# Performance work log

Hardware: AMD Instinct MI355X
Metric: run time of the kernel (lower is better)

The kernel has to match this reference:

```python
import jax, jax.numpy as jnp
import numpy as np

B, S, H = 1, 2048, 2048
NH = 16
HS = H // NH  # 128
NEG = -65504.0  # fp16 min used as additive mask value


def setup_inputs() -> dict:
    key = jax.random.key(0)
    k1, k2, k3, k4, k5 = jax.random.split(key, 5)
    hidden_states = jax.random.normal(k1, (B, S, H), dtype=jnp.float32)
    # causal left-to-right mask: 1 where attention allowed
    ltor_mask = jnp.tril(jnp.ones((S, S), dtype=jnp.float32))[None, None, :, :]
    W_qkv = jax.random.normal(k2, (H, 3 * H), dtype=jnp.float32) * (1.0 / np.sqrt(H))
    b_qkv = jax.random.normal(k3, (3 * H,), dtype=jnp.float32) * 0.01
    W_dense = jax.random.normal(k4, (H, H), dtype=jnp.float32) * (1.0 / np.sqrt(H))
    b_dense = jax.random.normal(k5, (H,), dtype=jnp.float32) * 0.01
    return {"hidden_states": hidden_states, "ltor_mask": ltor_mask,
            "W_qkv": W_qkv, "b_qkv": b_qkv, "W_dense": W_dense, "b_dense": b_dense}


def reference(hidden_states, ltor_mask, W_qkv, b_qkv, W_dense, b_dense):
    b, s, h = hidden_states.shape
    # fused QKV projection, then split along last dim (matches split_tensor_along_last_dim)
    qkv = hidden_states @ W_qkv + b_qkv  # [b, s, 3h]
    q, k, v = jnp.split(qkv, 3, axis=-1)
    q = q.reshape(b, s, NH, HS)
    k = k.reshape(b, s, NH, HS)
    v = v.reshape(b, s, NH, HS)
    scale = 1.0 / np.sqrt(HS)  # softmax_scale=None -> 1/sqrt(headdim)
    scores = jnp.einsum('bqhd,bkhd->bhqk', q, k) * scale
    scores = scores + NEG * (1.0 - ltor_mask)  # additive mask, [b,1,s,s] broadcast over heads
    probs = jax.nn.softmax(scores, axis=-1)
    ctx = jnp.einsum('bhqk,bkhd->bqhd', probs, v).reshape(b, s, h)
    out = ctx @ W_dense + b_dense  # output_dropout is identity in eval
    return out
```

## Files before the change

### kernel.cpp

```cpp
#include <hip/hip_runtime.h>
#include <math.h>

#define S_LEN 2048
#define HDIM  2048
#define NHEAD 16
#define HSZ   128
#define H3    6144

typedef __attribute__((ext_vector_type(8))) short bf16x8;
typedef __attribute__((ext_vector_type(4))) float f32x4;

__device__ inline ushort f2bf(float f) {
    union { float f; unsigned u; } c; c.f = f;
    unsigned u = c.u;
    return (ushort)((u + 0x7fffu + ((u >> 16) & 1u)) >> 16);
}
__device__ inline ushort f2bf_trunc(float f) {
    union { float f; unsigned u; } c; c.f = f;
    return (ushort)(c.u >> 16);
}

__global__ __launch_bounds__(256) void prep(
    const float* __restrict__ X,    ushort* __restrict__ Xb,
    const float* __restrict__ Wqkv, ushort* __restrict__ Wqt,
    const float* __restrict__ Wd,   ushort* __restrict__ Wdt)
{
    __shared__ ushort t[64][66];
    const int bid = blockIdx.x;
    const int tid = threadIdx.x;

    if (bid < 4096) {
        int i = bid * 1024 + tid * 4;
        float4 v = *(const float4*)(X + i);
        ushort4 o;
        o.x = f2bf(v.x); o.y = f2bf(v.y); o.z = f2bf(v.z); o.w = f2bf(v.w);
        *(ushort4*)(Xb + i) = o;
        return;
    }

    const float* W; ushort* Wt; int K, N, n0, k0;
    if (bid < 7168) {
        const int b = bid - 4096;
        W = Wqkv; Wt = Wqt; K = HDIM; N = H3;
        n0 = (b % 96) * 64; k0 = (b / 96) * 64;
    } else {
        const int b = bid - 7168;
        W = Wd; Wt = Wdt; K = HDIM; N = HDIM;
        n0 = (b % 32) * 64; k0 = (b / 32) * 64;
    }
    const int tx = tid & 15;
    const int ty = tid >> 4;
    #pragma unroll
    for (int p = 0; p < 4; p++) {
        const int k = p * 16 + ty;
        float4 v = *(const float4*)(&W[(size_t)(k0 + k) * N + n0 + tx * 4]);
        t[k][tx * 4 + 0] = f2bf(v.x);
        t[k][tx * 4 + 1] = f2bf(v.y);
        t[k][tx * 4 + 2] = f2bf(v.z);
        t[k][tx * 4 + 3] = f2bf(v.w);
    }
    __syncthreads();
    #pragma unroll
    for (int p = 0; p < 4; p++) {
        const int n = p * 16 + ty;
        ushort4 o;
        o.x = t[tx * 4 + 0][n];
        o.y = t[tx * 4 + 1][n];
        o.z = t[tx * 4 + 2][n];
        o.w = t[tx * 4 + 3][n];
        *(ushort4*)(&Wt[(size_t)(n0 + n) * K + k0 + tx * 4]) = o;
    }
}

__global__ __launch_bounds__(256) void transpose_v(const ushort* __restrict__ qkvb,
                                                   ushort* __restrict__ Vtb) {
    __shared__ ushort t[64][66];
    const int s0 = blockIdx.x * 64;
    const int d0 = blockIdx.y * 64;
    const int tx = threadIdx.x & 15;
    const int ty = threadIdx.x >> 4;
    #pragma unroll
    for (int p = 0; p < 4; p++) {
        const int s = p * 16 + ty;
        ushort4 v = *(const ushort4*)(&qkvb[(size_t)(s0 + s) * H3 + 2 * HDIM + d0 + tx * 4]);
        *(ushort4*)(&t[s][tx * 4]) = v;
    }
    __syncthreads();
    #pragma unroll
    for (int p = 0; p < 4; p++) {
        const int d = p * 16 + ty;
        ushort4 o;
        o.x = t[tx * 4 + 0][d];
        o.y = t[tx * 4 + 1][d];
        o.z = t[tx * 4 + 2][d];
        o.w = t[tx * 4 + 3][d];
        *(ushort4*)(&Vtb[(size_t)(d0 + d) * S_LEN + s0 + tx * 4]) = o;
    }
}

template <bool BF16_OUT>
__global__ __launch_bounds__(256) void gemm_bt_bias(
    const ushort* __restrict__ A, const ushort* __restrict__ Bt,
    const float* __restrict__ bias, float* __restrict__ C,
    ushort* __restrict__ Cb, int M, int N, int K)
{
    __shared__ ushort sA[2 * 128 * 32];
    __shared__ ushort sB[2 * 128 * 32];

    const int tid  = threadIdx.x;
    const int m0   = blockIdx.y * 128;
    const int n0   = blockIdx.x * 128;
    const int w    = tid >> 6;
    const int lane = tid & 63;
    const int quad = lane >> 4;
    const int l16  = lane & 15;
    const int wr   = (w >> 1) * 64;
    const int wc   = (w & 1) * 64;

    f32x4 acc[4][4] = {};

    for (int k0 = 0; k0 < K; k0 += 64) {
        #pragma unroll
        for (int iss = 0; iss < 4; iss++) {
            const int li  = iss * 256 + tid;
            const int c   = li >> 9;
            const int row = (li >> 2) & 127;
            const int kc  = (li & 3) * 8;
            const ushort* ga = A  + (size_t)(m0 + row) * K + k0 + c * 32 + kc;
            const ushort* gb = Bt + (size_t)(n0 + row) * K + k0 + c * 32 + kc;
            __builtin_amdgcn_global_load_lds(
                (const __attribute__((address_space(1))) void*)ga,
                (__attribute__((address_space(3))) void*)(sA + li * 8), 16, 0, 0);
            __builtin_amdgcn_global_load_lds(
                (const __attribute__((address_space(1))) void*)gb,
                (__attribute__((address_space(3))) void*)(sB + li * 8), 16, 0, 0);
        }
        __syncthreads();

        #pragma unroll
        for (int c = 0; c < 2; c++) {
            bf16x8 af[4], bq[4];
            #pragma unroll
            for (int i = 0; i < 4; i++)
                af[i] = *(const bf16x8*)(sA + c * 4096 + (wr + i * 16 + l16) * 32 + quad * 8);
            #pragma unroll
            for (int j = 0; j < 4; j++)
                bq[j] = *(const bf16x8*)(sB + c * 4096 + (wc + j * 16 + l16) * 32 + quad * 8);

            #pragma unroll
            for (int i = 0; i < 4; i++)
                #pragma unroll
                for (int j = 0; j < 4; j++)
                    acc[i][j] = __builtin_amdgcn_mfma_f32_16x16x32_bf16(
                        af[i], bq[j], acc[i][j], 0, 0, 0);
        }
        __syncthreads();
    }

    #pragma unroll
    for (int i = 0; i < 4; i++) {
        #pragma unroll
        for (int r = 0; r < 4; r++) {
            const int m = m0 + wr + i * 16 + quad * 4 + r;
            #pragma unroll
            for (int j = 0; j < 4; j++) {
                const int n = n0 + wc + j * 16 + l16;
                float v = acc[i][j][r] + bias[n];
                if (BF16_OUT) {
                    float vp = __shfl_xor(v, 1, 64);
                    unsigned both = (unsigned)f2bf(v) | ((unsigned)f2bf(vp) << 16);
                    if ((l16 & 1) == 0)
                        *(unsigned*)(Cb + (size_t)m * N + n) = both;
                } else {
                    C[(size_t)m * N + n] = v;
                }
            }
        }
    }
}

__global__ __launch_bounds__(256) void gemm_dense(
    const ushort* __restrict__ A, const ushort* __restrict__ Bt,
    const float* __restrict__ bias, float* __restrict__ C)
{
    __shared__ ushort sA[2 * 64 * 32];
    __shared__ ushort sB[2 * 128 * 32];

    const int tid  = threadIdx.x;
    const int m0   = blockIdx.y * 64;
    const int n0   = blockIdx.x * 128;
    const int w    = tid >> 6;
    const int lane = tid & 63;
    const int quad = lane >> 4;
    const int l16  = lane & 15;
    const int wr   = (w >> 1) * 32;
    const int wc   = (w & 1) * 64;

    f32x4 acc[2][4] = {};

    for (int k0 = 0; k0 < HDIM; k0 += 64) {
        #pragma unroll
        for (int iss = 0; iss < 2; iss++) {
            const int li  = iss * 256 + tid;
            const int c   = li >> 8;
            const int row = (li >> 2) & 63;
            const int kc  = (li & 3) * 8;
            const ushort* ga = A + (size_t)(m0 + row) * HDIM + k0 + c * 32 + kc;
            __builtin_amdgcn_global_load_lds(
                (const __attribute__((address_space(1))) void*)ga,
                (__attribute__((address_space(3))) void*)(sA + li * 8), 16, 0, 0);
        }
        #pragma unroll
        for (int iss = 0; iss < 4; iss++) {
            const int li  = iss * 256 + tid;
            const int c   = li >> 9;
            const int row = (li >> 2) & 127;
            const int kc  = (li & 3) * 8;
            const ushort* gb = Bt + (size_t)(n0 + row) * HDIM + k0 + c * 32 + kc;
            __builtin_amdgcn_global_load_lds(
                (const __attribute__((address_space(1))) void*)gb,
                (__attribute__((address_space(3))) void*)(sB + li * 8), 16, 0, 0);
        }
        __syncthreads();

        #pragma unroll
        for (int c = 0; c < 2; c++) {
            bf16x8 af[2], bq[4];
            #pragma unroll
            for (int i = 0; i < 2; i++)
                af[i] = *(const bf16x8*)(sA + c * 2048 + (wr + i * 16 + l16) * 32 + quad * 8);
            #pragma unroll
            for (int j = 0; j < 4; j++)
                bq[j] = *(const bf16x8*)(sB + c * 4096 + (wc + j * 16 + l16) * 32 + quad * 8);

            #pragma unroll
            for (int i = 0; i < 2; i++)
                #pragma unroll
                for (int j = 0; j < 4; j++)
                    acc[i][j] = __builtin_amdgcn_mfma_f32_16x16x32_bf16(
                        af[i], bq[j], acc[i][j], 0, 0, 0);
        }
        __syncthreads();
    }

    #pragma unroll
    for (int i = 0; i < 2; i++)
        #pragma unroll
        for (int r = 0; r < 4; r++) {
            const int m = m0 + wr + i * 16 + quad * 4 + r;
            #pragma unroll
            for (int j = 0; j < 4; j++) {
                const int n = n0 + wc + j * 16 + l16;
                C[(size_t)m * HDIM + n] = acc[i][j][r] + bias[n];
            }
        }
}

__global__ __launch_bounds__(256) void attn_mfma(
    const ushort* __restrict__ qkvb, const ushort* __restrict__ Vtb,
    ushort* __restrict__ ctxb)
{
    __shared__ __align__(16) ushort sK [2][64 * 128];
    __shared__ __align__(16) ushort sVt[2][128 * 64];
    __shared__ __align__(16) ushort Ps [4 * 1024];

    const int tid  = threadIdx.x;
    const int bid  = blockIdx.x;
    const int h    = bid & 15;
    const int qt   = (bid < 256) ? (31 - (bid >> 4)) : ((bid - 256) >> 4);
    const int q0   = qt * 64;
    const int w    = tid >> 6;
    const int lane = tid & 63;
    const int quad = lane >> 4;
    const int l16  = lane & 15;
    const int qr0  = q0 + w * 16;

    const float scale = 0.08838834764831845f;

    bf16x8 qf[4];
    #pragma unroll
    for (int c = 0; c < 4; c++)
        qf[c] = *(const bf16x8*)(qkvb + (size_t)(qr0 + l16) * H3 + h * HSZ + c * 32 + quad * 8);

    f32x4 o[8] = {};
    float lsum[4] = {0.f, 0.f, 0.f, 0.f};

    const int nt   = qt + 1;
    const int skey = tid >> 2;
    const int sq8  = tid & 3;

    auto stage = [&](int kt, int b) {
        const int k0 = kt * 64;
        #pragma unroll
        for (int iss = 0; iss < 4; iss++) {
            const int li = iss * 256 + tid;
            const ushort* g = qkvb + (size_t)(k0 + skey) * H3 + HDIM + h * HSZ + iss * 32 + sq8 * 8;
            __builtin_amdgcn_global_load_lds(
                (const __attribute__((address_space(1))) void*)g,
                (__attribute__((address_space(3))) void*)(&sK[b][0] + li * 8), 16, 0, 0);
        }
        #pragma unroll
        for (int iss = 0; iss < 4; iss++) {
            const int li = iss * 256 + tid;
            const int c  = li >> 9;
            const int d  = (li >> 2) & 127;
            const ushort* g = Vtb + (size_t)(h * HSZ + d) * S_LEN + k0 + c * 32 + (li & 3) * 8;
            __builtin_amdgcn_global_load_lds(
                (const __attribute__((address_space(1))) void*)g,
                (__attribute__((address_space(3))) void*)(&sVt[b][0] + li * 8), 16, 0, 0);
        }
    };

    stage(0, 0);
    const int wofs = w * 1024;

    for (int kt = 0; kt < nt; kt++) {
        const int b  = kt & 1;
        const int k0 = kt * 64;

        if (kt + 1 < nt) {
            stage(kt + 1, b ^ 1);
            asm volatile("s_waitcnt vmcnt(8)" ::: "memory");
        } else {
            asm volatile("s_waitcnt vmcnt(0)" ::: "memory");
        }
        asm volatile("s_barrier" ::: "memory");

        const ushort* bK = &sK[b][0];
        const ushort* bV = &sVt[b][0];

        f32x4 sacc[4] = {};
        #pragma unroll
        for (int jt = 0; jt < 4; jt++)
            #pragma unroll
            for (int c = 0; c < 4; c++) {
                bf16x8 kf = *(const bf16x8*)(bK + c * 2048 + (jt * 16 + l16) * 32 + quad * 8);
                sacc[jt] = __builtin_amdgcn_mfma_f32_16x16x32_bf16(qf[c], kf, sacc[jt], 0, 0, 0);
            }

        float p[4][4];
        if (kt == nt - 1) {
            #pragma unroll
            for (int jt = 0; jt < 4; jt++) {
                const int key = k0 + jt * 16 + l16;
                #pragma unroll
                for (int r = 0; r < 4; r++) {
                    float e = __expf(sacc[jt][r] * scale);
                    if (key > qr0 + quad * 4 + r) e = 0.f;
                    p[jt][r] = e;
                    lsum[r] += e;
                }
            }
        } else {
            #pragma unroll
            for (int jt = 0; jt < 4; jt++)
                #pragma unroll
                for (int r = 0; r < 4; r++) {
                    float e = __expf(sacc[jt][r] * scale);
                    p[jt][r] = e;
                    lsum[r] += e;
                }
        }

        #pragma unroll
        for (int jt = 0; jt < 4; jt++) {
            const int cpan = jt >> 1;
            const int lch  = (jt & 1) * 2 + (l16 >> 3);
            const int phys = lch ^ quad;
            #pragma unroll
            for (int r = 0; r < 4; r++) {
                const int row = quad * 4 + r;
                Ps[wofs + cpan * 512 + row * 32 + phys * 8 + (l16 & 7)] = f2bf_trunc(p[jt][r]);
            }
        }

        #pragma unroll
        for (int c = 0; c < 2; c++) {
            const int pph = quad ^ (l16 >> 2);
            bf16x8 pf = *(const bf16x8*)(Ps + wofs + c * 512 + l16 * 32 + pph * 8);
            #pragma unroll
            for (int ht = 0; ht < 8; ht++) {
                bf16x8 vf = *(const bf16x8*)(bV + c * 4096 + (ht * 16 + l16) * 32 + quad * 8);
                o[ht] = __builtin_amdgcn_mfma_f32_16x16x32_bf16(pf, vf, o[ht], 0, 0, 0);
            }
        }

        asm volatile("s_waitcnt lgkmcnt(0)" ::: "memory");
        asm volatile("s_barrier" ::: "memory");
    }

    float invl[4];
    #pragma unroll
    for (int r = 0; r < 4; r++) {
        float ls = lsum[r];
        #pragma unroll
        for (int off = 1; off < 16; off <<= 1)
            ls += __shfl_xor(ls, off, 64);
        invl[r] = 1.0f / ls;
    }
    #pragma unroll
    for (int ht = 0; ht < 8; ht++) {
        #pragma unroll
        for (int r = 0; r < 4; r++) {
            float v  = o[ht][r] * invl[r];
            float vp = __shfl_xor(v, 1, 64);
            unsigned both = (unsigned)f2bf(v) | ((unsigned)f2bf(vp) << 16);
            if ((l16 & 1) == 0)
                *(unsigned*)(ctxb + (size_t)(qr0 + quad * 4 + r) * HDIM + h * HSZ + ht * 16 + l16) = both;
        }
    }
}

extern "C" void kernel_launch(void* const* d_in, const int* in_sizes, int n_in,
                              void* d_out, int out_size, void* d_ws, size_t ws_size,
                              hipStream_t stream) {
    const float* X    = (const float*)d_in[0];
    const float* Wqkv = (const float*)d_in[2];
    const float* bqkv = (const float*)d_in[3];
    const float* Wd   = (const float*)d_in[4];
    const float* bd   = (const float*)d_in[5];
    float* out = (float*)d_out;

    ushort* Xb   = (ushort*)d_ws;
    ushort* Wqt  = Xb   + (size_t)S_LEN * HDIM;
    ushort* Wdt  = Wqt  + (size_t)H3 * HDIM;
    ushort* ctxb = Wdt  + (size_t)HDIM * HDIM;
    ushort* qkvb = ctxb + (size_t)S_LEN * HDIM;
    ushort* Vtb  = qkvb + (size_t)S_LEN * H3;

    dim3 blk(256);

    prep<<<dim3(8192), blk, 0, stream>>>(X, Xb, Wqkv, Wqt, Wd, Wdt);

    gemm_bt_bias<true><<<dim3(H3 / 128, S_LEN / 128), blk, 0, stream>>>(
        Xb, Wqt, bqkv, nullptr, qkvb, S_LEN, H3, HDIM);

    transpose_v<<<dim3(S_LEN / 64, HDIM / 64), blk, 0, stream>>>(qkvb, Vtb);

    attn_mfma<<<dim3(512), blk, 0, stream>>>(qkvb, Vtb, ctxb);

    gemm_dense<<<dim3(HDIM / 128, S_LEN / 64), blk, 0, stream>>>(
        ctxb, Wdt, bd, out);
}
```

Baseline: 288.0 us.

## Rewrite QKV GEMM with 256x256 tiles, double-buffered swizzled LDS and ping-pong MFMA

Replaces the 128x128 QKV projection GEMM with a 512-thread kernel that computes 256x256 output tiles using 64-wide K steps. Loads are double-buffered through direct global-to-LDS copies with an XOR swizzle to avoid bank conflicts, and waits use explicit vmcnt and barriers. The MFMA work is split into quadrant phases interleaved with LDS fragment loads, with s_setprio raised around the MFMA bursts. The goal is more data reuse per loaded byte and overlap of loads with compute. The trade-off is only 192 blocks, fewer than the CU count, and 128KB of LDS per block, which limits occupancy.

After: 287.6 us. Within noise of the previous version (-0.1%).

```diff
diff --git a/kernel.cpp b/kernel.cpp
--- a/kernel.cpp
+++ b/kernel.cpp
@@ -98,82 +98,156 @@
     }
 }
 
-template <bool BF16_OUT>
-__global__ __launch_bounds__(256) void gemm_bt_bias(
+__global__ __launch_bounds__(512, 2) void gemm_qkv_256(
     const ushort* __restrict__ A, const ushort* __restrict__ Bt,
-    const float* __restrict__ bias, float* __restrict__ C,
-    ushort* __restrict__ Cb, int M, int N, int K)
+    const float* __restrict__ bias, ushort* __restrict__ Cb,
+    int M, int N, int K)
 {
-    __shared__ ushort sA[2 * 128 * 32];
-    __shared__ ushort sB[2 * 128 * 32];
+    __shared__ __align__(16) ushort lds[2][2 * 256 * 64];
 
     const int tid  = threadIdx.x;
-    const int m0   = blockIdx.y * 128;
-    const int n0   = blockIdx.x * 128;
+    const int m0   = blockIdx.y * 256;
+    const int n0   = blockIdx.x * 256;
     const int w    = tid >> 6;
+    const int wm   = w >> 2;
+    const int wn   = w & 3;
     const int lane = tid & 63;
     const int quad = lane >> 4;
     const int l16  = lane & 15;
-    const int wr   = (w >> 1) * 64;
-    const int wc   = (w & 1) * 64;
-
-    f32x4 acc[4][4] = {};
-
-    for (int k0 = 0; k0 < K; k0 += 64) {
-        #pragma unroll
-        for (int iss = 0; iss < 4; iss++) {
-            const int li  = iss * 256 + tid;
-            const int c   = li >> 9;
-            const int row = (li >> 2) & 127;
-            const int kc  = (li & 3) * 8;
-            const ushort* ga = A  + (size_t)(m0 + row) * K + k0 + c * 32 + kc;
-            const ushort* gb = Bt + (size_t)(n0 + row) * K + k0 + c * 32 + kc;
+
+    const int csw   = ((tid & 7) ^ ((tid >> 3) & 7)) * 8;
+    const int rbase = tid >> 3;
+    const int rdsw  = l16 & 7;
+
+    f32x4 acc[8][4] = {};
+
+    const int T = K / 64;
+
+    auto stage = [&](int kt, int b) {
+        const int k0 = kt * 64;
+        #pragma unroll
+        for (int r = 0; r < 4; r++) {
+            const int row = r * 64 + rbase;
+            const ushort* ga = A + (size_t)(m0 + row) * K + k0 + csw;
             __builtin_amdgcn_global_load_lds(
                 (const __attribute__((address_space(1))) void*)ga,
-                (__attribute__((address_space(3))) void*)(sA + li * 8), 16, 0, 0);
+                (__attribute__((address_space(3))) void*)(&lds[b][0] + (r * 512 + tid) * 8), 16, 0, 0);
+        }
+        #pragma unroll
+        for (int r = 0; r < 4; r++) {
+            const int row = r * 64 + rbase;
+            const ushort* gb = Bt + (size_t)(n0 + row) * K + k0 + csw;
             __builtin_amdgcn_global_load_lds(
                 (const __attribute__((address_space(1))) void*)gb,
-                (__attribute__((address_space(3))) void*)(sB + li * 8), 16, 0, 0);
-        }
-        __syncthreads();
-
-        #pragma unroll
-        for (int c = 0; c < 2; c++) {
-            bf16x8 af[4], bq[4];
-            #pragma unroll
-            for (int i = 0; i < 4; i++)
-                af[i] = *(const bf16x8*)(sA + c * 4096 + (wr + i * 16 + l16) * 32 + quad * 8);
-            #pragma unroll
-            for (int j = 0; j < 4; j++)
-                bq[j] = *(const bf16x8*)(sB + c * 4096 + (wc + j * 16 + l16) * 32 + quad * 8);
-
-            #pragma unroll
-            for (int i = 0; i < 4; i++)
-                #pragma unroll
-                for (int j = 0; j < 4; j++)
+                (__attribute__((address_space(3))) void*)(&lds[b][16384] + (r * 512 + tid) * 8), 16, 0, 0);
+        }
+    };
+
+    stage(0, 0);
+
+    for (int t = 0; t < T; t++) {
+        const int b = t & 1;
+        if (t + 1 < T) {
+            stage(t + 1, b ^ 1);
+            asm volatile("s_waitcnt vmcnt(8)" ::: "memory");
+        } else {
+            asm volatile("s_waitcnt vmcnt(0)" ::: "memory");
+        }
+        asm volatile("s_barrier" ::: "memory");
+
+        const ushort* bA = &lds[b][0];
+        const ushort* bB = &lds[b][16384];
+
+        bf16x8 af[4][2], bqa[2][2], bqb[2][2];
+
+        #pragma unroll
+        for (int i = 0; i < 4; i++)
+            #pragma unroll
+            for (int kc = 0; kc < 2; kc++)
+                af[i][kc] = *(const bf16x8*)(bA + (wm * 128 + i * 16 + l16) * 64
+                                               + ((((kc << 2) | quad) ^ rdsw) * 8));
+        #pragma unroll
+        for (int j = 0; j < 2; j++)
+            #pragma unroll
+            for (int kc = 0; kc < 2; kc++)
+                bqa[j][kc] = *(const bf16x8*)(bB + (wn * 64 + j * 16 + l16) * 64
+                                                + ((((kc << 2) | quad) ^ rdsw) * 8));
+        asm volatile("s_barrier" ::: "memory");
+        __builtin_amdgcn_s_setprio(1);
+        #pragma unroll
+        for (int i = 0; i < 4; i++)
+            #pragma unroll
+            for (int j = 0; j < 2; j++)
+                #pragma unroll
+                for (int kc = 0; kc < 2; kc++)
                     acc[i][j] = __builtin_amdgcn_mfma_f32_16x16x32_bf16(
-                        af[i], bq[j], acc[i][j], 0, 0, 0);
-        }
-        __syncthreads();
-    }
-
-    #pragma unroll
-    for (int i = 0; i < 4; i++) {
+                        af[i][kc], bqa[j][kc], acc[i][j], 0, 0, 0);
+        __builtin_amdgcn_s_setprio(0);
+        asm volatile("s_barrier" ::: "memory");
+
+        #pragma unroll
+        for (int j = 0; j < 2; j++)
+            #pragma unroll
+            for (int kc = 0; kc < 2; kc++)
+                bqb[j][kc] = *(const bf16x8*)(bB + (wn * 64 + (2 + j) * 16 + l16) * 64
+                                                + ((((kc << 2) | quad) ^ rdsw) * 8));
+        asm volatile("s_barrier" ::: "memory");
+        __builtin_amdgcn_s_setprio(1);
+        #pragma unroll
+        for (int i = 0; i < 4; i++)
+            #pragma unroll
+            for (int j = 0; j < 2; j++)
+                #pragma unroll
+                for (int kc = 0; kc < 2; kc++)
+                    acc[i][2 + j] = __builtin_amdgcn_mfma_f32_16x16x32_bf16(
+                        af[i][kc], bqb[j][kc], acc[i][2 + j], 0, 0, 0);
+        __builtin_amdgcn_s_setprio(0);
+        asm volatile("s_barrier" ::: "memory");
+
+        #pragma unroll
+        for (int i = 0; i < 4; i++)
+            #pragma unroll
+            for (int kc = 0; kc < 2; kc++)
+                af[i][kc] = *(const bf16x8*)(bA + (wm * 128 + (4 + i) * 16 + l16) * 64
+                                               + ((((kc << 2) | quad) ^ rdsw) * 8));
+        asm volatile("s_barrier" ::: "memory");
+        __builtin_amdgcn_s_setprio(1);
+        #pragma unroll
+        for (int i = 0; i < 4; i++)
+            #pragma unroll
+            for (int j = 0; j < 2; j++)
+                #pragma unroll
+                for (int kc = 0; kc < 2; kc++)
+                    acc[4 + i][2 + j] = __builtin_amdgcn_mfma_f32_16x16x32_bf16(
+                        af[i][kc], bqb[j][kc], acc[4 + i][2 + j], 0, 0, 0);
+        __builtin_amdgcn_s_setprio(0);
+        asm volatile("s_barrier" ::: "memory");
+
+        __builtin_amdgcn_s_setprio(1);
+        #pragma unroll
+        for (int i = 0; i < 4; i++)
+            #pragma unroll
+            for (int j = 0; j < 2; j++)
+                #pragma unroll
+                for (int kc = 0; kc < 2; kc++)
+                    acc[4 + i][j] = __builtin_amdgcn_mfma_f32_16x16x32_bf16(
+                        af[i][kc], bqa[j][kc], acc[4 + i][j], 0, 0, 0);
+        __builtin_amdgcn_s_setprio(0);
+    }
+
+    #pragma unroll
+    for (int i = 0; i < 8; i++) {
         #pragma unroll
         for (int r = 0; r < 4; r++) {
-            const int m = m0 + wr + i * 16 + quad * 4 + r;
+            const int m = m0 + wm * 128 + i * 16 + quad * 4 + r;
             #pragma unroll
             for (int j = 0; j < 4; j++) {
-                const int n = n0 + wc + j * 16 + l16;
-                float v = acc[i][j][r] + bias[n];
-                if (BF16_OUT) {
-                    float vp = __shfl_xor(v, 1, 64);
-                    unsigned both = (unsigned)f2bf(v) | ((unsigned)f2bf(vp) << 16);
-                    if ((l16 & 1) == 0)
-                        *(unsigned*)(Cb + (size_t)m * N + n) = both;
-                } else {
-                    C[(size_t)m * N + n] = v;
-                }
+                const int n = n0 + wn * 64 + j * 16 + l16;
+                float v  = acc[i][j][r] + bias[n];
+                float vp = __shfl_xor(v, 1, 64);
+                unsigned both = (unsigned)f2bf(v) | ((unsigned)f2bf(vp) << 16);
+                if ((l16 & 1) == 0)
+                    *(unsigned*)(Cb + (size_t)m * N + n) = both;
             }
         }
     }
@@ -432,8 +506,8 @@
 
     prep<<<dim3(8192), blk, 0, stream>>>(X, Xb, Wqkv, Wqt, Wd, Wdt);
 
-    gemm_bt_bias<true><<<dim3(H3 / 128, S_LEN / 128), blk, 0, stream>>>(
-        Xb, Wqt, bqkv, nullptr, qkvb, S_LEN, H3, HDIM);
+    gemm_qkv_256<<<dim3(H3 / 256, S_LEN / 256), dim3(512), 0, stream>>>(
+        Xb, Wqt, bqkv, qkvb, S_LEN, H3, HDIM);
 
     transpose_v<<<dim3(S_LEN / 64, HDIM / 64), blk, 0, stream>>>(qkvb, Vtb);
 
```
